# Kernel optimization log

Hardware: AMD Instinct MI355X
Metric: run time of the kernel (lower is better)

## Reference

```python
import jax, jax.numpy as jnp
import numpy as np

N, T, S, D = 2, 16, 196, 768
HEADS = 12
SCALE = (D // HEADS) ** -0.5  # 0.125


def setup_inputs() -> dict:
    key = jax.random.key(0)
    k1, k2, k3, k4 = jax.random.split(key, 4)
    x = jax.random.normal(k1, (N, T, S, D), dtype=jnp.float32)
    # torch Linear(dim, 3*dim, bias=False): store as [D, 3D] for x @ W
    W_qkv = jax.random.normal(k2, (D, 3 * D), dtype=jnp.float32) * (D ** -0.5)
    W_proj = jax.random.normal(k3, (D, D), dtype=jnp.float32) * (D ** -0.5)
    b_proj = jax.random.normal(k4, (D,), dtype=jnp.float32) * 0.02
    return {"x": x, "W_qkv": W_qkv, "W_proj": W_proj, "b_proj": b_proj}


def reference(x, W_qkv, W_proj, b_proj):
    n, t, s, d = x.shape
    hd = d // HEADS
    qkv = x @ W_qkv                      # [N,T,S,3D]
    q, k, v = jnp.split(qkv, 3, axis=-1)
    # subsample_func: spatial stride-2 subsampling of K and V
    k = k[:, :, ::2, :]                  # [N,T,S//2,D]
    v = v[:, :, ::2, :]
    q4 = q.reshape(n, -1, HEADS, hd)     # [N, Q=T*S, H, hd]
    k4 = k.reshape(n, -1, HEADS, hd)     # [N, K=T*ceil(S/2), H, hd]
    v4 = v.reshape(n, -1, HEADS, hd)
    attn = jnp.einsum('nqhd,nkhd->nqkh', q4, k4) * SCALE
    attn = jax.nn.softmax(attn, axis=2)  # softmax over k (dim=-2)
    out = jnp.einsum('nqkh,nkhd->nqhd', attn, v4)
    out = out.reshape(n, t, s, d)
    return out @ W_proj + b_proj
```

## Files before the change

kernel.cpp:

```cpp
#include <hip/hip_runtime.h>
#include <hip/hip_bf16.h>

#define NB 2
#define TT 16
#define SS 196
#define DD 768
#define NHEADS 12
#define HD 64
#define TOK (NB*TT*SS)
#define QPN (TT*SS)
#define KPN (TT*(SS/2))

typedef _Float16 f16;
typedef _Float16 f16x4 __attribute__((ext_vector_type(4)));
typedef _Float16 f16x8 __attribute__((ext_vector_type(8)));
typedef float    f32x4 __attribute__((ext_vector_type(4)));
typedef unsigned int u32;

static __device__ __forceinline__ u32 pk16(float a, float b) {
    return __builtin_bit_cast(u32, __builtin_amdgcn_cvt_pkrtz(a, b));
}

__global__ void cast_f32_to_f16(const float* __restrict__ in, f16* __restrict__ out, int n4) {
    int i = blockIdx.x * blockDim.x + threadIdx.x;
    if (i < n4) {
        float4 v = reinterpret_cast<const float4*>(in)[i];
        f16x4 h; h[0] = (f16)v.x; h[1] = (f16)v.y; h[2] = (f16)v.z; h[3] = (f16)v.w;
        reinterpret_cast<f16x4*>(out)[i] = h;
    }
}

__global__ void transpose_cast(const float* __restrict__ in, f16* __restrict__ out, int R, int C) {
    __shared__ float tile[32][33];
    int c0 = blockIdx.x * 32, r0 = blockIdx.y * 32;
    int tx = threadIdx.x & 31, ty = threadIdx.x >> 5;
#pragma unroll
    for (int j = 0; j < 4; j++)
        tile[ty + 8*j][tx] = in[(size_t)(r0 + ty + 8*j) * C + c0 + tx];
    __syncthreads();
#pragma unroll
    for (int j = 0; j < 4; j++)
        out[(size_t)(c0 + ty + 8*j) * R + r0 + tx] = (f16)tile[tx][ty + 8*j];
}

template<int EPI>
__launch_bounds__(256, 2)
__global__ void gemm_f16(const f16* __restrict__ A, const f16* __restrict__ Bt,
                         int M, int N, int K,
                         f16* __restrict__ q16, f16* __restrict__ k16,
                         f16* __restrict__ vt16,
                         const float* __restrict__ bias, float* __restrict__ outf) {
    __shared__ f16 As[128 * 40];
    __shared__ f16 Bs[128 * 40];
    int tid  = threadIdx.x;
    int lane = tid & 63, w = tid >> 6;
    int wm = w >> 1, wn = w & 1;
    int l15 = lane & 15, l4 = lane >> 4;
    int mBase = blockIdx.y * 128, nBase = blockIdx.x * 128;
    int r0 = tid >> 2, s0 = tid & 3;

    f32x4 acc[4][4] = {};

    const int KT = K / 32;
    for (int kt = 0; kt < KT; kt++) {
        int k0 = kt * 32;
        *(f16x8*)&As[r0*40 + s0*8]        = *(const f16x8*)&A [(size_t)(mBase + r0     ) * K + k0 + s0*8];
        *(f16x8*)&As[(r0+64)*40 + s0*8]   = *(const f16x8*)&A [(size_t)(mBase + r0 + 64) * K + k0 + s0*8];
        *(f16x8*)&Bs[r0*40 + s0*8]        = *(const f16x8*)&Bt[(size_t)(nBase + r0     ) * K + k0 + s0*8];
        *(f16x8*)&Bs[(r0+64)*40 + s0*8]   = *(const f16x8*)&Bt[(size_t)(nBase + r0 + 64) * K + k0 + s0*8];
        __syncthreads();
        f16x8 af[4], bf[4];
#pragma unroll
        for (int i = 0; i < 4; i++) {
            af[i] = *(const f16x8*)&As[(wm*64 + i*16 + l15)*40 + l4*8];
            bf[i] = *(const f16x8*)&Bs[(wn*64 + i*16 + l15)*40 + l4*8];
        }
#pragma unroll
        for (int i = 0; i < 4; i++)
#pragma unroll
            for (int j = 0; j < 4; j++)
                acc[i][j] = __builtin_amdgcn_mfma_f32_16x16x32_f16(af[i], bf[j], acc[i][j], 0, 0, 0);
        __syncthreads();
    }

    int rbase2 = mBase + wm*64;
    int cbase2 = nBase + wn*64;
#pragma unroll
    for (int i = 0; i < 4; i++) {
#pragma unroll
        for (int j = 0; j < 4; j++) {
            int col = cbase2 + j*16 + l15;
#pragma unroll
            for (int r = 0; r < 4; r++) {
                int row = rbase2 + i*16 + l4*4 + r;
                float val = acc[i][j][r];
                if constexpr (EPI == 0) {
                    if (col < 768) {
                        q16[(size_t)row * 768 + col] = (f16)(val * 0.125f);
                    } else {
                        int n = row / QPN; int rem = row - n*QPN;
                        int t = rem / SS;  int s   = rem - t*SS;
                        if (!(s & 1)) {
                            int kb = t*(SS/2) + (s >> 1);
                            if (col < 1536) {
                                k16[(size_t)(n*KPN + kb) * 768 + (col - 768)] = (f16)val;
                            } else {
                                int c = col - 1536; int hh = c >> 6, dd = c & 63;
                                vt16[((size_t)(n*NHEADS + hh)*64 + dd) * KPN + kb] = (f16)val;
                            }
                        }
                    }
                } else {
                    outf[(size_t)row * 768 + col] = val + bias[col];
                }
            }
        }
    }
}

__launch_bounds__(256, 2)
__global__ void attn_mfma(const f16* __restrict__ q16, const f16* __restrict__ k16,
                          const f16* __restrict__ vt16, f16* __restrict__ o16) {
    int tid = threadIdx.x;
    int lane = tid & 63, w = tid >> 6;
    int qt = blockIdx.x, nh = blockIdx.y;
    int n = nh / NHEADS, h = nh - n*NHEADS;
    int l15 = lane & 15, l4 = lane >> 4;

    __shared__ f16 Klds[32 * 64];
    __shared__ f16 Vtlds[64 * 40];
    __shared__ f16 Plds[4][16 * 40];

    int krow = tid >> 3, kseg = tid & 7;
    u32 kwo = (u32)((krow * 128 + kseg * 16) ^ ((krow & 7) << 4));
    int vd = tid >> 2, vseg = tid & 3;

    const f16* kgb = k16 + (size_t)n * KPN * 768 + h * 64;
    const f16* vgb = vt16 + ((size_t)nh * 64 + vd) * KPN;

    int qglob = n*QPN + qt*64 + w*16 + l15;
    const f16* qrow = q16 + (size_t)qglob * 768 + h*64;
    f16x8 qf0 = *(const f16x8*)&qrow[l4*8];
    f16x8 qf1 = *(const f16x8*)&qrow[32 + l4*8];

    f32x4 acc[4] = {};
    float M = -INFINITY, L = 0.f;

    f16x8 stK = *(const f16x8*)&kgb[(size_t)krow * 768 + kseg*8];
    f16x8 stV = *(const f16x8*)&vgb[vseg*8];

    for (int t = 0; t < 49; t++) {
        __syncthreads();
        *(f16x8*)((char*)Klds + kwo) = stK;
        *(f16x8*)&Vtlds[vd*40 + vseg*8] = stV;
        __syncthreads();

        if (t < 48) {
            int kb = (t + 1) * 32;
            stK = *(const f16x8*)&kgb[(size_t)(kb + krow) * 768 + kseg*8];
            stV = *(const f16x8*)&vgb[kb + vseg*8];
        }

        f32x4 S0 = {}, S1 = {};
#pragma unroll
        for (int kh = 0; kh < 2; kh++) {
            int rowb = (kh*16 + l15) * 128;
            u32 x = (u32)((l15 & 7) << 4);
            f16x8 ka0 = *(const f16x8*)((char*)Klds + ((rowb +      l4*16) ^ x));
            f16x8 ka1 = *(const f16x8*)((char*)Klds + ((rowb + 64 + l4*16) ^ x));
            f32x4& S = kh ? S1 : S0;
            S = __builtin_amdgcn_mfma_f32_16x16x32_f16(ka0, qf0, S, 0, 0, 0);
            S = __builtin_amdgcn_mfma_f32_16x16x32_f16(ka1, qf1, S, 0, 0, 0);
        }

        float tm = fmaxf(fmaxf(fmaxf(S0[0], S0[1]), fmaxf(S0[2], S0[3])),
                         fmaxf(fmaxf(S1[0], S1[1]), fmaxf(S1[2], S1[3])));
        tm = fmaxf(tm, __shfl_xor(tm, 16));
        tm = fmaxf(tm, __shfl_xor(tm, 32));
        float Mnew = fmaxf(M, tm);
        float cor = __expf(M - Mnew);
        float ls;
        f16* pw = &Plds[w][l15*40];
        {
            float p0 = __expf(S0[0]-Mnew), p1 = __expf(S0[1]-Mnew);
            float p2 = __expf(S0[2]-Mnew), p3 = __expf(S0[3]-Mnew);
            float p4 = __expf(S1[0]-Mnew), p5 = __expf(S1[1]-Mnew);
            float p6 = __expf(S1[2]-Mnew), p7 = __expf(S1[3]-Mnew);
            ls = ((p0+p1)+(p2+p3)) + ((p4+p5)+(p6+p7));
            uint2 pkA; pkA.x = pk16(p0, p1); pkA.y = pk16(p2, p3);
            *(uint2*)&pw[l4*4] = pkA;
            uint2 pkB; pkB.x = pk16(p4, p5); pkB.y = pk16(p6, p7);
            *(uint2*)&pw[16 + l4*4] = pkB;
        }
        ls += __shfl_xor(ls, 16);
        ls += __shfl_xor(ls, 32);
        L = L * cor + ls;
        M = Mnew;
#pragma unroll
        for (int c = 0; c < 4; c++) acc[c] *= cor;

        f16x8 pf = *(const f16x8*)&Plds[w][l15*40 + l4*8];
#pragma unroll
        for (int c = 0; c < 4; c++) {
            f16x8 vf = *(const f16x8*)((char*)Vtlds + (c*16 + l15)*80 + l4*16);
            acc[c] = __builtin_amdgcn_mfma_f32_16x16x32_f16(vf, pf, acc[c], 0, 0, 0);
        }
    }

    float inv = 1.f / L;
    f16* orow = o16 + (size_t)qglob * 768 + h*64;
#pragma unroll
    for (int c = 0; c < 4; c++) {
        uint2 o2;
        o2.x = pk16(acc[c][0]*inv, acc[c][1]*inv);
        o2.y = pk16(acc[c][2]*inv, acc[c][3]*inv);
        *(uint2*)&orow[c*16 + l4*4] = o2;
    }
}

extern "C" void kernel_launch(void* const* d_in, const int* in_sizes, int n_in,
                              void* d_out, int out_size, void* d_ws, size_t ws_size,
                              hipStream_t stream) {
    const float* x      = (const float*)d_in[0];
    const float* W_qkv  = (const float*)d_in[1];
    const float* W_proj = (const float*)d_in[2];
    const float* b_proj = (const float*)d_in[3];
    float* out = (float*)d_out;

    char* ws = (char*)d_ws;
    size_t off = 0;
    auto alloc = [&](size_t bytes) { void* p = ws + off; off += (bytes + 255) & ~255ULL; return p; };
    f16* x16    = (f16*)alloc((size_t)TOK * DD * 2);
    f16* WqkvT  = (f16*)alloc((size_t)2304 * 768 * 2);
    f16* WprojT = (f16*)alloc((size_t)768 * 768 * 2);
    f16* q16    = (f16*)alloc((size_t)TOK * DD * 2);
    f16* k16    = (f16*)alloc((size_t)NB * KPN * DD * 2);
    f16* vt16   = (f16*)alloc((size_t)NB * NHEADS * HD * KPN * 2);
    f16* o16    = (f16*)alloc((size_t)TOK * DD * 2);
    (void)ws_size; (void)in_sizes; (void)n_in; (void)out_size;

    cast_f32_to_f16<<<(TOK*DD/4 + 255)/256, 256, 0, stream>>>(x, x16, TOK*DD/4);
    transpose_cast<<<dim3(2304/32, 768/32), 256, 0, stream>>>(W_qkv, WqkvT, 768, 2304);
    transpose_cast<<<dim3(768/32, 768/32), 256, 0, stream>>>(W_proj, WprojT, 768, 768);
    gemm_f16<0><<<dim3(2304/128, 6272/128), 256, 0, stream>>>(
        x16, WqkvT, TOK, 2304, 768, q16, k16, vt16, nullptr, nullptr);
    attn_mfma<<<dim3(49, 24), 256, 0, stream>>>(q16, k16, vt16, o16);
    gemm_f16<1><<<dim3(768/128, 6272/128), 256, 0, stream>>>(
        o16, WprojT, TOK, 768, 768, nullptr, nullptr, nullptr, b_proj, out);
}
```

Before: 226.4 us.

## Widen attention K/V tiles to 64 keys with lazy softmax rescaling

Raises the attention kernel's key tile from 32 to 64 keys per iteration, with a 32-key tail tile processed after the loop, which halves the number of barrier-synchronized iterations. The running max is only updated when the new tile max exceeds it by more than 8 (wave-uniform check), so the rescaling of accumulators is skipped in most iterations. LDS layout changes from an XOR swizzle to padded rows of stride 68. The trade-offs are higher register and LDS use, possible bank conflicts from the new padding, and somewhat larger fp16 probability values under the lazy threshold.

```diff
diff --git a/kernel.cpp b/kernel.cpp
--- a/kernel.cpp
+++ b/kernel.cpp
@@ -127,16 +127,15 @@
     int n = nh / NHEADS, h = nh - n*NHEADS;
     int l15 = lane & 15, l4 = lane >> 4;
 
-    __shared__ f16 Klds[32 * 64];
-    __shared__ f16 Vtlds[64 * 40];
-    __shared__ f16 Plds[4][16 * 40];
-
-    int krow = tid >> 3, kseg = tid & 7;
-    u32 kwo = (u32)((krow * 128 + kseg * 16) ^ ((krow & 7) << 4));
-    int vd = tid >> 2, vseg = tid & 3;
-
+    __shared__ f16 Klds[64 * 68];
+    __shared__ f16 Vtlds[64 * 68];
+    __shared__ f16 Plds[4][16 * 68];
+
+    int srow = tid >> 3, sseg = tid & 7;
     const f16* kgb = k16 + (size_t)n * KPN * 768 + h * 64;
-    const f16* vgb = vt16 + ((size_t)nh * 64 + vd) * KPN;
+    const f16* vgb = vt16 + ((size_t)nh * 64 + srow) * KPN;
+    int tvd = tid >> 2, tvs = tid & 3;
+    const f16* vgb_tail = vt16 + ((size_t)nh * 64 + tvd) * KPN;
 
     int qglob = n*QPN + qt*64 + w*16 + l15;
     const f16* qrow = q16 + (size_t)qglob * 768 + h*64;
@@ -146,63 +145,129 @@
     f32x4 acc[4] = {};
     float M = -INFINITY, L = 0.f;
 
-    f16x8 stK = *(const f16x8*)&kgb[(size_t)krow * 768 + kseg*8];
-    f16x8 stV = *(const f16x8*)&vgb[vseg*8];
-
-    for (int t = 0; t < 49; t++) {
+    f16x8 stKa = *(const f16x8*)&kgb[(size_t)srow * 768 + sseg*8];
+    f16x8 stKb = *(const f16x8*)&kgb[(size_t)(srow+32) * 768 + sseg*8];
+    f16x8 stVa = *(const f16x8*)&vgb[sseg*8];
+    f16x8 stVb = *(const f16x8*)&vgb[(size_t)32*KPN + sseg*8];
+
+    for (int t = 0; t < 24; t++) {
         __syncthreads();
-        *(f16x8*)((char*)Klds + kwo) = stK;
-        *(f16x8*)&Vtlds[vd*40 + vseg*8] = stV;
+        *(f16x8*)&Klds [srow*68 + sseg*8]      = stKa;
+        *(f16x8*)&Klds [(srow+32)*68 + sseg*8] = stKb;
+        *(f16x8*)&Vtlds[srow*68 + sseg*8]      = stVa;
+        *(f16x8*)&Vtlds[(srow+32)*68 + sseg*8] = stVb;
         __syncthreads();
 
-        if (t < 48) {
-            int kb = (t + 1) * 32;
-            stK = *(const f16x8*)&kgb[(size_t)(kb + krow) * 768 + kseg*8];
-            stV = *(const f16x8*)&vgb[kb + vseg*8];
-        }
-
-        f32x4 S0 = {}, S1 = {};
-#pragma unroll
-        for (int kh = 0; kh < 2; kh++) {
-            int rowb = (kh*16 + l15) * 128;
-            u32 x = (u32)((l15 & 7) << 4);
-            f16x8 ka0 = *(const f16x8*)((char*)Klds + ((rowb +      l4*16) ^ x));
-            f16x8 ka1 = *(const f16x8*)((char*)Klds + ((rowb + 64 + l4*16) ^ x));
-            f32x4& S = kh ? S1 : S0;
-            S = __builtin_amdgcn_mfma_f32_16x16x32_f16(ka0, qf0, S, 0, 0, 0);
-            S = __builtin_amdgcn_mfma_f32_16x16x32_f16(ka1, qf1, S, 0, 0, 0);
-        }
-
-        float tm = fmaxf(fmaxf(fmaxf(S0[0], S0[1]), fmaxf(S0[2], S0[3])),
-                         fmaxf(fmaxf(S1[0], S1[1]), fmaxf(S1[2], S1[3])));
+        if (t < 23) {
+            int kb = (t + 1) * 64;
+            stKa = *(const f16x8*)&kgb[(size_t)(kb + srow) * 768 + sseg*8];
+            stKb = *(const f16x8*)&kgb[(size_t)(kb + srow + 32) * 768 + sseg*8];
+            stVa = *(const f16x8*)&vgb[kb + sseg*8];
+            stVb = *(const f16x8*)&vgb[(size_t)32*KPN + kb + sseg*8];
+        } else {
+            stKa = *(const f16x8*)&kgb[(size_t)(1536 + srow) * 768 + sseg*8];
+            stVa = *(const f16x8*)&vgb_tail[1536 + tvs*8];
+        }
+
+        f32x4 S[4];
+#pragma unroll
+        for (int kh = 0; kh < 4; kh++) {
+            const f16* kr = &Klds[(kh*16 + l15)*68];
+            f16x8 ka0 = *(const f16x8*)&kr[l4*8];
+            f16x8 ka1 = *(const f16x8*)&kr[32 + l4*8];
+            f32x4 s = {};
+            s = __builtin_amdgcn_mfma_f32_16x16x32_f16(ka0, qf0, s, 0, 0, 0);
+            s = __builtin_amdgcn_mfma_f32_16x16x32_f16(ka1, qf1, s, 0, 0, 0);
+            S[kh] = s;
+        }
+
+        float tm = -INFINITY;
+#pragma unroll
+        for (int kh = 0; kh < 4; kh++)
+            tm = fmaxf(tm, fmaxf(fmaxf(S[kh][0], S[kh][1]), fmaxf(S[kh][2], S[kh][3])));
         tm = fmaxf(tm, __shfl_xor(tm, 16));
         tm = fmaxf(tm, __shfl_xor(tm, 32));
-        float Mnew = fmaxf(M, tm);
-        float cor = __expf(M - Mnew);
-        float ls;
-        f16* pw = &Plds[w][l15*40];
-        {
-            float p0 = __expf(S0[0]-Mnew), p1 = __expf(S0[1]-Mnew);
-            float p2 = __expf(S0[2]-Mnew), p3 = __expf(S0[3]-Mnew);
-            float p4 = __expf(S1[0]-Mnew), p5 = __expf(S1[1]-Mnew);
-            float p6 = __expf(S1[2]-Mnew), p7 = __expf(S1[3]-Mnew);
-            ls = ((p0+p1)+(p2+p3)) + ((p4+p5)+(p6+p7));
-            uint2 pkA; pkA.x = pk16(p0, p1); pkA.y = pk16(p2, p3);
-            *(uint2*)&pw[l4*4] = pkA;
-            uint2 pkB; pkB.x = pk16(p4, p5); pkB.y = pk16(p6, p7);
-            *(uint2*)&pw[16 + l4*4] = pkB;
+        if (!__all(tm - M <= 8.f)) {
+            float Mnew = fmaxf(M, tm);
+            float cor = __expf(M - Mnew);
+            L *= cor;
+#pragma unroll
+            for (int c = 0; c < 4; c++) acc[c] *= cor;
+            M = Mnew;
+        }
+        float ls = 0.f;
+        f16* pw = &Plds[w][l15*68];
+#pragma unroll
+        for (int kh = 0; kh < 4; kh++) {
+            float p0 = __expf(S[kh][0] - M), p1 = __expf(S[kh][1] - M);
+            float p2 = __expf(S[kh][2] - M), p3 = __expf(S[kh][3] - M);
+            ls += (p0 + p1) + (p2 + p3);
+            uint2 pk2; pk2.x = pk16(p0, p1); pk2.y = pk16(p2, p3);
+            *(uint2*)&pw[kh*16 + l4*4] = pk2;
         }
         ls += __shfl_xor(ls, 16);
         ls += __shfl_xor(ls, 32);
-        L = L * cor + ls;
-        M = Mnew;
-#pragma unroll
-        for (int c = 0; c < 4; c++) acc[c] *= cor;
-
-        f16x8 pf = *(const f16x8*)&Plds[w][l15*40 + l4*8];
+        L += ls;
+
+#pragma unroll
+        for (int ks = 0; ks < 2; ks++) {
+            f16x8 pf = *(const f16x8*)&Plds[w][l15*68 + ks*32 + l4*8];
+#pragma unroll
+            for (int c = 0; c < 4; c++) {
+                f16x8 vf = *(const f16x8*)&Vtlds[(c*16 + l15)*68 + ks*32 + l4*8];
+                acc[c] = __builtin_amdgcn_mfma_f32_16x16x32_f16(vf, pf, acc[c], 0, 0, 0);
+            }
+        }
+    }
+
+    __syncthreads();
+    *(f16x8*)&Klds [srow*68 + sseg*8] = stKa;
+    *(f16x8*)&Vtlds[tvd*68 + tvs*8]   = stVa;
+    __syncthreads();
+    {
+        f32x4 S[2];
+#pragma unroll
+        for (int kh = 0; kh < 2; kh++) {
+            const f16* kr = &Klds[(kh*16 + l15)*68];
+            f16x8 ka0 = *(const f16x8*)&kr[l4*8];
+            f16x8 ka1 = *(const f16x8*)&kr[32 + l4*8];
+            f32x4 s = {};
+            s = __builtin_amdgcn_mfma_f32_16x16x32_f16(ka0, qf0, s, 0, 0, 0);
+            s = __builtin_amdgcn_mfma_f32_16x16x32_f16(ka1, qf1, s, 0, 0, 0);
+            S[kh] = s;
+        }
+        float tm = -INFINITY;
+#pragma unroll
+        for (int kh = 0; kh < 2; kh++)
+            tm = fmaxf(tm, fmaxf(fmaxf(S[kh][0], S[kh][1]), fmaxf(S[kh][2], S[kh][3])));
+        tm = fmaxf(tm, __shfl_xor(tm, 16));
+        tm = fmaxf(tm, __shfl_xor(tm, 32));
+        if (!__all(tm - M <= 8.f)) {
+            float Mnew = fmaxf(M, tm);
+            float cor = __expf(M - Mnew);
+            L *= cor;
+#pragma unroll
+            for (int c = 0; c < 4; c++) acc[c] *= cor;
+            M = Mnew;
+        }
+        float ls = 0.f;
+        f16* pw = &Plds[w][l15*68];
+#pragma unroll
+        for (int kh = 0; kh < 2; kh++) {
+            float p0 = __expf(S[kh][0] - M), p1 = __expf(S[kh][1] - M);
+            float p2 = __expf(S[kh][2] - M), p3 = __expf(S[kh][3] - M);
+            ls += (p0 + p1) + (p2 + p3);
+            uint2 pk2; pk2.x = pk16(p0, p1); pk2.y = pk16(p2, p3);
+            *(uint2*)&pw[kh*16 + l4*4] = pk2;
+        }
+        ls += __shfl_xor(ls, 16);
+        ls += __shfl_xor(ls, 32);
+        L += ls;
+
+        f16x8 pf = *(const f16x8*)&Plds[w][l15*68 + l4*8];
 #pragma unroll
         for (int c = 0; c < 4; c++) {
-            f16x8 vf = *(const f16x8*)((char*)Vtlds + (c*16 + l15)*80 + l4*16);
+            f16x8 vf = *(const f16x8*)&Vtlds[(c*16 + l15)*68 + l4*8];
             acc[c] = __builtin_amdgcn_mfma_f32_16x16x32_f16(vf, pf, acc[c], 0, 0, 0);
         }
     }
```

After: 307.2 us. +35.7%, slower.
